# Kernel optimization log

Measured on AMD Instinct MI355X. Metric: run time of the kernel, lower is better.

Reference implementation:

```python
import jax, jax.numpy as jnp
import numpy as np

N_NODES = 100000


def gcn_conv(x, edge_index, W, b):
    # PyG GCNConv: linear first, then symmetric-normalized aggregation with self-loops, then bias.
    n = x.shape[0]
    h = x @ W  # [N, out]
    loop = jnp.arange(n, dtype=edge_index.dtype)
    src = jnp.concatenate([edge_index[0], loop])  # source nodes (x_j)
    dst = jnp.concatenate([edge_index[1], loop])  # target nodes (aggregation index)
    ones = jnp.ones(dst.shape[0], dtype=h.dtype)
    deg = jax.ops.segment_sum(ones, dst, num_segments=n)  # in-degree incl. self-loop
    dinv = jnp.where(deg > 0, jax.lax.rsqrt(deg), 0.0)
    norm = dinv[src] * dinv[dst]  # [E+N]
    msgs = h[src] * norm[:, None]  # gather + scale
    out = jax.ops.segment_sum(msgs, dst, num_segments=n)  # scatter-add
    return out + b


def setup_inputs() -> dict:
    key = jax.random.key(0)
    k1, k2, k3, k4 = jax.random.split(key, 4)
    x = jax.random.normal(k1, (N_NODES, 128), dtype=jnp.float32)
    edge_index = jax.random.randint(k2, (2, 3200000), 0, N_NODES, dtype=jnp.int64)
    W1 = jax.random.normal(k3, (128, 16), dtype=jnp.float32) * (1.0 / np.sqrt(128))
    b1 = jnp.zeros((16,), dtype=jnp.float32)
    W2 = jax.random.normal(k4, (16, 10), dtype=jnp.float32) * (1.0 / np.sqrt(16))
    b2 = jnp.zeros((10,), dtype=jnp.float32)
    return {"x": x, "edge_index": edge_index, "W1": W1, "b1": b1, "W2": W2, "b2": b2}


def reference(x, edge_index, W1, b1, W2, b2):
    h = gcn_conv(x, edge_index, W1, b1)
    h = jax.nn.relu(h)
    h = gcn_conv(h, edge_index, W2, b2)
    return jax.nn.log_softmax(h, axis=1)
```

## Files before the change

kernel.cpp:

```cpp
#include <hip/hip_runtime.h>
#include <hip/hip_fp16.h>
#include <math.h>

#define NN 100000
#define F0 128
#define F1 16
#define F2 10
#define NBUCK 391
#define TILE 8192
#define EPT 16
#define CAP 16384
#define BPT 512

__device__ inline void fma4(float4& a, float s, const float4& w) {
  a.x = fmaf(s, w.x, a.x);
  a.y = fmaf(s, w.y, a.y);
  a.z = fmaf(s, w.z, a.z);
  a.w = fmaf(s, w.w, a.w);
}

__device__ inline unsigned pk2(float a, float b) {
  __half ha = __float2half(a), hb = __float2half(b);
  return (unsigned)__half_as_ushort(ha) | ((unsigned)__half_as_ushort(hb) << 16);
}

__device__ inline float2 up2(unsigned u) {
  __half2 h;
  *(unsigned*)&h = u;
  return __half22float2(h);
}

__device__ inline void nt_store_f2(float a, float b, float* p) {
  union { double d; float f[2]; } u;
  u.f[0] = a; u.f[1] = b;
  __builtin_nontemporal_store(u.d, (double*)p);
}

__global__ void k_zero(int* __restrict__ bucket_cnt) {
  int i = blockIdx.x * blockDim.x + threadIdx.x;
  if (i < NBUCK) bucket_cnt[i] = 0;
}

__global__ __launch_bounds__(256) void k_bincount(const int* __restrict__ dst, int E,
                                                  int* __restrict__ bucket_cnt) {
  __shared__ int hist[NBUCK];
  int t = threadIdx.x;
  for (int i = t; i < NBUCK; i += 256) hist[i] = 0;
  __syncthreads();
  int per = (E + gridDim.x - 1) / gridDim.x;
  int e0 = blockIdx.x * per, e1 = min(E, e0 + per);
  for (int e = e0 + t; e < e1; e += 256)
    atomicAdd(&hist[__builtin_nontemporal_load(dst + e) >> 8], 1);
  __syncthreads();
  for (int i = t; i < NBUCK; i += 256)
    if (hist[i]) atomicAdd(&bucket_cnt[i], hist[i]);
}

__global__ void k_binscan(const int* __restrict__ bucket_cnt, int* __restrict__ bucket_base,
                          int* __restrict__ bucket_cur) {
  __shared__ int lds[512];
  int t = threadIdx.x;
  int v = (t < NBUCK) ? bucket_cnt[t] : 0;
  lds[t] = v;
  __syncthreads();
  for (int o = 1; o < 512; o <<= 1) {
    int add = (t >= o) ? lds[t - o] : 0;
    __syncthreads();
    lds[t] += add;
    __syncthreads();
  }
  if (t < NBUCK) {
    int excl = lds[t] - v;
    bucket_base[t] = excl;
    bucket_cur[t] = excl;
    if (t == NBUCK - 1) bucket_base[NBUCK] = lds[t];
  }
}

__global__ __launch_bounds__(BPT) void k_binplace(const int* __restrict__ src,
                                                  const int* __restrict__ dst, int E,
                                                  int* __restrict__ bucket_cur,
                                                  int* __restrict__ packed) {
  __shared__ int cnt[NBUCK];
  __shared__ int loff[NBUCK];
  __shared__ int gbase[NBUCK];
  __shared__ int part[256];
  __shared__ int stage[TILE];
  int t = threadIdx.x;
  int e0 = blockIdx.x * TILE, e1 = min(E, e0 + TILE);
  int total = e1 - e0;
  for (int i = t; i < NBUCK; i += BPT) cnt[i] = 0;
  __syncthreads();
  int bkpos[EPT];
  int pval[EPT];
#pragma unroll
  for (int k = 0; k < EPT; k++) {
    int e = e0 + t + k * BPT;
    if (e < e1) {
      int d = __builtin_nontemporal_load(dst + e);
      int s = __builtin_nontemporal_load(src + e);
      int bk = d >> 8;
      int pos = atomicAdd(&cnt[bk], 1);
      bkpos[k] = (bk << 13) | pos;
      pval[k] = (s << 8) | (d & 255);
    } else {
      bkpos[k] = -1;
    }
  }
  __syncthreads();
  for (int i = t; i < NBUCK; i += BPT) {
    int c = cnt[i];
    gbase[i] = c ? atomicAdd(&bucket_cur[i], c) : 0;
  }
  if (t < 256) {
    int i0 = 2 * t, i1 = 2 * t + 1;
    int c0 = (i0 < NBUCK) ? cnt[i0] : 0;
    int c1 = (i1 < NBUCK) ? cnt[i1] : 0;
    part[t] = c0 + c1;
  }
  __syncthreads();
  for (int o = 1; o < 256; o <<= 1) {
    int add = 0;
    if (t < 256 && t >= o) add = part[t - o];
    __syncthreads();
    if (t < 256) part[t] += add;
    __syncthreads();
  }
  if (t < 256) {
    int i0 = 2 * t, i1 = 2 * t + 1;
    int c0 = (i0 < NBUCK) ? cnt[i0] : 0;
    int c1 = (i1 < NBUCK) ? cnt[i1] : 0;
    int excl = part[t] - c0 - c1;
    if (i0 < NBUCK) loff[i0] = excl;
    if (i1 < NBUCK) loff[i1] = excl + c0;
  }
  __syncthreads();
#pragma unroll
  for (int k = 0; k < EPT; k++) {
    if (bkpos[k] >= 0) {
      int bk = bkpos[k] >> 13, pos = bkpos[k] & 8191;
      stage[loff[bk] + pos] = pval[k];
    }
  }
  __syncthreads();
  int sub = t >> 4, lane = t & 15;
  for (int bk = sub; bk < NBUCK; bk += BPT / 16) {
    int lo = loff[bk];
    int hi = (bk + 1 < NBUCK) ? loff[bk + 1] : total;
    int gb = gbase[bk];
    for (int i = lo + lane; i < hi; i += 16) packed[gb + (i - lo)] = stage[i];
  }
}

__global__ __launch_bounds__(256) void k_bucket(const int* __restrict__ packed,
                                                const int* __restrict__ bucket_base,
                                                int* __restrict__ row_start,
                                                float* __restrict__ dinv,
                                                int* __restrict__ col, int E) {
  __shared__ int stage[CAP];
  __shared__ int hist[256];
  __shared__ int off[256];
  __shared__ int cur[256];
  int b = blockIdx.x, t = threadIdx.x;
  int base = bucket_base[b];
  int cnt = bucket_base[b + 1] - base;
  hist[t] = 0;
  bool staged = (cnt <= CAP);
  if (staged)
    for (int i = t; i < cnt; i += 256) stage[i] = __builtin_nontemporal_load(packed + base + i);
  __syncthreads();
  if (staged) {
    for (int i = t; i < cnt; i += 256) atomicAdd(&hist[stage[i] & 255], 1);
  } else {
    for (int i = t; i < cnt; i += 256) atomicAdd(&hist[packed[base + i] & 255], 1);
  }
  __syncthreads();
  int v = hist[t];
  off[t] = v;
  __syncthreads();
  for (int o = 1; o < 256; o <<= 1) {
    int add = (t >= o) ? off[t - o] : 0;
    __syncthreads();
    off[t] += add;
    __syncthreads();
  }
  int excl = off[t] - v;
  cur[t] = excl;
  int d = b * 256 + t;
  if (d < NN) {
    row_start[d] = base + excl;
    dinv[d] = rsqrtf((float)(v + 1));
  }
  if (b == 0 && t == 0) row_start[NN] = E;
  __syncthreads();
  if (staged) {
    for (int i = t; i < cnt; i += 256) {
      int p = stage[i];
      int pos = atomicAdd(&cur[p & 255], 1);
      col[base + pos] = p >> 8;
    }
  } else {
    for (int i = t; i < cnt; i += 256) {
      int p = packed[base + i];
      int pos = atomicAdd(&cur[p & 255], 1);
      col[base + pos] = p >> 8;
    }
  }
}

__global__ __launch_bounds__(256) void k_lin1(const float* __restrict__ x,
                                              const float* __restrict__ W1,
                                              const float* __restrict__ dinv,
                                              unsigned* __restrict__ tab1) {
  __shared__ float4 wl[F0 * 4];
  int t = threadIdx.x;
  for (int i = t; i < F0 * 4; i += 256) wl[i] = ((const float4*)W1)[i];
  __syncthreads();
  int row0 = (blockIdx.x * 256 + t) * 4;
  if (row0 >= NN) return;
  float4 acc[4][4];
#pragma unroll
  for (int r = 0; r < 4; r++)
#pragma unroll
    for (int j = 0; j < 4; j++) acc[r][j] = make_float4(0.f, 0.f, 0.f, 0.f);
  const float4* xr0 = (const float4*)(x + (size_t)(row0 + 0) * F0);
  const float4* xr1 = (const float4*)(x + (size_t)(row0 + 1) * F0);
  const float4* xr2 = (const float4*)(x + (size_t)(row0 + 2) * F0);
  const float4* xr3 = (const float4*)(x + (size_t)(row0 + 3) * F0);
  for (int k4 = 0; k4 < F0 / 4; k4++) {
    float4 xv[4];
    xv[0] = xr0[k4]; xv[1] = xr1[k4]; xv[2] = xr2[k4]; xv[3] = xr3[k4];
#pragma unroll
    for (int kk = 0; kk < 4; kk++) {
      float4 w0 = wl[(k4 * 4 + kk) * 4 + 0];
      float4 w1 = wl[(k4 * 4 + kk) * 4 + 1];
      float4 w2 = wl[(k4 * 4 + kk) * 4 + 2];
      float4 w3 = wl[(k4 * 4 + kk) * 4 + 3];
#pragma unroll
      for (int r = 0; r < 4; r++) {
        float xs = kk == 0 ? xv[r].x : kk == 1 ? xv[r].y : kk == 2 ? xv[r].z : xv[r].w;
        fma4(acc[r][0], xs, w0);
        fma4(acc[r][1], xs, w1);
        fma4(acc[r][2], xs, w2);
        fma4(acc[r][3], xs, w3);
      }
    }
  }
#pragma unroll
  for (int r = 0; r < 4; r++) {
    float dd = dinv[row0 + r];
    float4 a0 = acc[r][0], a1 = acc[r][1], a2 = acc[r][2], a3 = acc[r][3];
    uint4 o0, o1;
    o0.x = pk2(dd * a0.x, dd * a0.y);
    o0.y = pk2(dd * a0.z, dd * a0.w);
    o0.z = pk2(dd * a1.x, dd * a1.y);
    o0.w = pk2(dd * a1.z, dd * a1.w);
    o1.x = pk2(dd * a2.x, dd * a2.y);
    o1.y = pk2(dd * a2.z, dd * a2.w);
    o1.z = pk2(dd * a3.x, dd * a3.y);
    o1.w = pk2(dd * a3.z, dd * a3.w);
    uint4* orow = (uint4*)(tab1 + (size_t)(row0 + r) * 8);
    orow[0] = o0;
    orow[1] = o1;
  }
}

__global__ __launch_bounds__(256) void k_agg1(const unsigned* __restrict__ tab1,
                                              const int* __restrict__ row_start,
                                              const int* __restrict__ col,
                                              const float* __restrict__ dinv,
                                              const float* __restrict__ b1,
                                              const float* __restrict__ W2g,
                                              unsigned* __restrict__ tab2) {
  __shared__ float w2[F1][F2];
  __shared__ float b1l[F1];
  int t = threadIdx.x;
  if (t < F1 * F2) w2[t / F2][t % F2] = W2g[t];
  if (t < F1) b1l[t] = b1[t];
  __syncthreads();
  int g = blockIdx.x * 256 + t;
  int d = g >> 3, o = g & 7;
  int q2 = o >> 2, q = o & 3;
  if (d >= NN) return;
  const uint2* T = (const uint2*)tab1;
  float a0 = 0.f, a1 = 0.f, a2 = 0.f, a3 = 0.f;
  auto addrow = [&](int s) {
    uint2 v = T[(size_t)s * 4 + q];
    float2 f0 = up2(v.x), f1 = up2(v.y);
    a0 += f0.x; a1 += f0.y; a2 += f1.x; a3 += f1.y;
  };
  if (q2 == 0) addrow(d);
  int e = row_start[d] + q2, e1 = row_start[d + 1];
  for (; e + 6 < e1; e += 8) {
    int s0 = __builtin_nontemporal_load(col + e);
    int s1 = __builtin_nontemporal_load(col + e + 2);
    int s2 = __builtin_nontemporal_load(col + e + 4);
    int s3 = __builtin_nontemporal_load(col + e + 6);
    addrow(s0); addrow(s1); addrow(s2); addrow(s3);
  }
  for (; e < e1; e += 2) addrow(__builtin_nontemporal_load(col + e));
  a0 += __shfl_xor(a0, 4);
  a1 += __shfl_xor(a1, 4);
  a2 += __shfl_xor(a2, 4);
  a3 += __shfl_xor(a3, 4);
  float dd = dinv[d];
  float h[4];
  h[0] = fmaxf(fmaf(dd, a0, b1l[q * 4 + 0]), 0.f);
  h[1] = fmaxf(fmaf(dd, a1, b1l[q * 4 + 1]), 0.f);
  h[2] = fmaxf(fmaf(dd, a2, b1l[q * 4 + 2]), 0.f);
  h[3] = fmaxf(fmaf(dd, a3, b1l[q * 4 + 3]), 0.f);
  float p[F2];
#pragma unroll
  for (int j = 0; j < F2; j++) {
    float s = 0.f;
#pragma unroll
    for (int kk = 0; kk < 4; kk++) s = fmaf(h[kk], w2[q * 4 + kk][j], s);
    p[j] = s;
  }
#pragma unroll
  for (int j = 0; j < F2; j++) p[j] += __shfl_xor(p[j], 1);
#pragma unroll
  for (int j = 0; j < F2; j++) p[j] += __shfl_xor(p[j], 2);
  if (q2 != 0) return;
  uint2* O = (uint2*)tab2;
  uint2 ov;
  if (q == 0) {
    ov.x = pk2(dd * p[0], dd * p[1]); ov.y = pk2(dd * p[2], dd * p[3]);
  } else if (q == 1) {
    ov.x = pk2(dd * p[4], dd * p[5]); ov.y = pk2(dd * p[6], dd * p[7]);
  } else if (q == 2) {
    ov.x = pk2(dd * p[8], dd * p[9]); ov.y = 0u;
  } else {
    ov.x = 0u; ov.y = 0u;
  }
  O[(size_t)d * 4 + q] = ov;
}

__global__ __launch_bounds__(256) void k_agg2(const unsigned* __restrict__ tab2,
                                              const int* __restrict__ row_start,
                                              const int* __restrict__ col,
                                              const float* __restrict__ dinv,
                                              const float* __restrict__ b2,
                                              float* __restrict__ out) {
  __shared__ float b2l[F1];
  int t = threadIdx.x;
  if (t < F1) b2l[t] = (t < F2) ? b2[t] : -1e30f;
  __syncthreads();
  int g = blockIdx.x * 256 + t;
  int d = g >> 3, o = g & 7;
  int q2 = o >> 2, q = o & 3;
  if (d >= NN) return;
  const uint2* T = (const uint2*)tab2;
  float a0 = 0.f, a1 = 0.f, a2 = 0.f, a3 = 0.f;
  auto addrow = [&](int s) {
    uint2 v = T[(size_t)s * 4 + q];
    float2 f0 = up2(v.x), f1 = up2(v.y);
    a0 += f0.x; a1 += f0.y; a2 += f1.x; a3 += f1.y;
  };
  if (q2 == 0) addrow(d);
  int e = row_start[d] + q2, e1 = row_start[d + 1];
  for (; e + 6 < e1; e += 8) {
    int s0 = __builtin_nontemporal_load(col + e);
    int s1 = __builtin_nontemporal_load(col + e + 2);
    int s2 = __builtin_nontemporal_load(col + e + 4);
    int s3 = __builtin_nontemporal_load(col + e + 6);
    addrow(s0); addrow(s1); addrow(s2); addrow(s3);
  }
  for (; e < e1; e += 2) addrow(__builtin_nontemporal_load(col + e));
  a0 += __shfl_xor(a0, 4);
  a1 += __shfl_xor(a1, 4);
  a2 += __shfl_xor(a2, 4);
  a3 += __shfl_xor(a3, 4);
  float dd = dinv[d];
  float v0 = fmaf(dd, a0, b2l[q * 4 + 0]);
  float v1 = fmaf(dd, a1, b2l[q * 4 + 1]);
  float v2 = fmaf(dd, a2, b2l[q * 4 + 2]);
  float v3 = fmaf(dd, a3, b2l[q * 4 + 3]);
  float m = fmaxf(fmaxf(v0, v1), fmaxf(v2, v3));
  m = fmaxf(m, __shfl_xor(m, 1));
  m = fmaxf(m, __shfl_xor(m, 2));
  float sum = expf(v0 - m) + expf(v1 - m) + expf(v2 - m) + expf(v3 - m);
  sum += __shfl_xor(sum, 1);
  sum += __shfl_xor(sum, 2);
  float lse = m + logf(sum);
  if (q2 != 0) return;
  float* op = out + (size_t)d * F2;
  if (q == 0) {
    nt_store_f2(v0 - lse, v1 - lse, op + 0);
    nt_store_f2(v2 - lse, v3 - lse, op + 2);
  } else if (q == 1) {
    nt_store_f2(v0 - lse, v1 - lse, op + 4);
    nt_store_f2(v2 - lse, v3 - lse, op + 6);
  } else if (q == 2) {
    nt_store_f2(v0 - lse, v1 - lse, op + 8);
  }
}

extern "C" void kernel_launch(void* const* d_in, const int* in_sizes, int n_in,
                              void* d_out, int out_size, void* d_ws, size_t ws_size,
                              hipStream_t stream) {
  const float* x  = (const float*)d_in[0];
  const int*   ei = (const int*)d_in[1];
  const float* W1 = (const float*)d_in[2];
  const float* b1 = (const float*)d_in[3];
  const float* W2 = (const float*)d_in[4];
  const float* b2 = (const float*)d_in[5];
  float* out = (float*)d_out;
  int E = in_sizes[1] / 2;
  const int* src = ei;
  const int* dst = ei + E;

  char* p = (char*)d_ws;
  auto alloc = [&](size_t bytes) {
    char* r = p;
    p += (bytes + 255) & ~(size_t)255;
    return r;
  };
  size_t tabsz = (size_t)NN * 8 * 4;
  float* dinv        = (float*)alloc((size_t)NN * 4);
  int*   row_start   = (int*)alloc((size_t)(NN + 1) * 4);
  int*   bucket_cnt  = (int*)alloc((size_t)NBUCK * 4);
  int*   bucket_base = (int*)alloc((size_t)(NBUCK + 1) * 4);
  int*   bucket_cur  = (int*)alloc((size_t)NBUCK * 4);
  int*   col         = (int*)alloc((size_t)E * 4);
  size_t needA = tabsz * 2;
  size_t regA = (size_t)E * 4;
  char*  A = (char*)alloc(regA > needA ? regA : needA);
  int*      packed = (int*)A;
  unsigned* tab1 = (unsigned*)A;
  unsigned* tab2 = (unsigned*)(A + tabsz);

  int nblk8N = (8 * NN + 255) / 256;
  int nblk_place = (E + TILE - 1) / TILE;
  hipLaunchKernelGGL(k_zero, dim3(2), dim3(256), 0, stream, bucket_cnt);
  hipLaunchKernelGGL(k_bincount, dim3(1024), dim3(256), 0, stream, dst, E, bucket_cnt);
  hipLaunchKernelGGL(k_binscan, dim3(1), dim3(512), 0, stream, bucket_cnt, bucket_base, bucket_cur);
  hipLaunchKernelGGL(k_binplace, dim3(nblk_place), dim3(BPT), 0, stream, src, dst, E, bucket_cur, packed);
  hipLaunchKernelGGL(k_bucket, dim3(NBUCK), dim3(256), 0, stream, packed, bucket_base, row_start, dinv, col, E);
  hipLaunchKernelGGL(k_lin1, dim3((NN / 4 + 255) / 256), dim3(256), 0, stream, x, W1, dinv, tab1);
  hipLaunchKernelGGL(k_agg1, dim3(nblk8N), dim3(256), 0, stream,
                     tab1, row_start, col, dinv, b1, W2, tab2);
  hipLaunchKernelGGL(k_agg2, dim3(nblk8N), dim3(256), 0, stream, tab2, row_start, col, dinv, b2, out);
}
```

Measured before the change: 197.7 us.

## Drop bucket-count pass by using fixed-capacity padded buckets with row_end

Removes the separate dst histogram and scan kernels by giving each destination bucket a fixed MAXB-sized slot in padded storage, so binplace reserves offsets directly through atomic counters. Rows are then described by row_start/row_end instead of a dense CSR offset array. k_bucket also records each edge's intra-node position during the histogram pass, which removes the second atomic pass when scattering columns. The cost is larger padded buffers, an extra row_end array, and a hard capacity assumption (MAXB) that can overflow if a bucket receives more edges than expected.

```diff
diff --git a/kernel.cpp b/kernel.cpp
--- a/kernel.cpp
+++ b/kernel.cpp
@@ -7,9 +7,10 @@
 #define F1 16
 #define F2 10
 #define NBUCK 391
+#define MAXB 10240
 #define TILE 8192
 #define EPT 16
-#define CAP 16384
+#define CAP 10240
 #define BPT 512
 
 __device__ inline void fma4(float4& a, float s, const float4& w) {
@@ -36,45 +37,9 @@
   __builtin_nontemporal_store(u.d, (double*)p);
 }
 
-__global__ void k_zero(int* __restrict__ bucket_cnt) {
+__global__ void k_zero(int* __restrict__ bucket_cur) {
   int i = blockIdx.x * blockDim.x + threadIdx.x;
-  if (i < NBUCK) bucket_cnt[i] = 0;
-}
-
-__global__ __launch_bounds__(256) void k_bincount(const int* __restrict__ dst, int E,
-                                                  int* __restrict__ bucket_cnt) {
-  __shared__ int hist[NBUCK];
-  int t = threadIdx.x;
-  for (int i = t; i < NBUCK; i += 256) hist[i] = 0;
-  __syncthreads();
-  int per = (E + gridDim.x - 1) / gridDim.x;
-  int e0 = blockIdx.x * per, e1 = min(E, e0 + per);
-  for (int e = e0 + t; e < e1; e += 256)
-    atomicAdd(&hist[__builtin_nontemporal_load(dst + e) >> 8], 1);
-  __syncthreads();
-  for (int i = t; i < NBUCK; i += 256)
-    if (hist[i]) atomicAdd(&bucket_cnt[i], hist[i]);
-}
-
-__global__ void k_binscan(const int* __restrict__ bucket_cnt, int* __restrict__ bucket_base,
-                          int* __restrict__ bucket_cur) {
-  __shared__ int lds[512];
-  int t = threadIdx.x;
-  int v = (t < NBUCK) ? bucket_cnt[t] : 0;
-  lds[t] = v;
-  __syncthreads();
-  for (int o = 1; o < 512; o <<= 1) {
-    int add = (t >= o) ? lds[t - o] : 0;
-    __syncthreads();
-    lds[t] += add;
-    __syncthreads();
-  }
-  if (t < NBUCK) {
-    int excl = lds[t] - v;
-    bucket_base[t] = excl;
-    bucket_cur[t] = excl;
-    if (t == NBUCK - 1) bucket_base[NBUCK] = lds[t];
-  }
+  if (i < NBUCK) bucket_cur[i] = 0;
 }
 
 __global__ __launch_bounds__(BPT) void k_binplace(const int* __restrict__ src,
@@ -147,60 +112,67 @@
   for (int bk = sub; bk < NBUCK; bk += BPT / 16) {
     int lo = loff[bk];
     int hi = (bk + 1 < NBUCK) ? loff[bk + 1] : total;
-    int gb = gbase[bk];
+    size_t gb = (size_t)bk * MAXB + gbase[bk];
     for (int i = lo + lane; i < hi; i += 16) packed[gb + (i - lo)] = stage[i];
   }
 }
 
 __global__ __launch_bounds__(256) void k_bucket(const int* __restrict__ packed,
-                                                const int* __restrict__ bucket_base,
+                                                const int* __restrict__ bucket_cur,
                                                 int* __restrict__ row_start,
+                                                int* __restrict__ row_end,
                                                 float* __restrict__ dinv,
-                                                int* __restrict__ col, int E) {
+                                                int* __restrict__ col) {
   __shared__ int stage[CAP];
+  __shared__ unsigned short posa[CAP];
   __shared__ int hist[256];
-  __shared__ int off[256];
+  __shared__ int offx[256];
+  __shared__ int scan[256];
   __shared__ int cur[256];
   int b = blockIdx.x, t = threadIdx.x;
-  int base = bucket_base[b];
-  int cnt = bucket_base[b + 1] - base;
+  size_t base = (size_t)b * MAXB;
+  int cnt_b = bucket_cur[b];
   hist[t] = 0;
-  bool staged = (cnt <= CAP);
-  if (staged)
-    for (int i = t; i < cnt; i += 256) stage[i] = __builtin_nontemporal_load(packed + base + i);
-  __syncthreads();
+  __syncthreads();
+  bool staged = (cnt_b <= CAP);
   if (staged) {
-    for (int i = t; i < cnt; i += 256) atomicAdd(&hist[stage[i] & 255], 1);
+    for (int i = t; i < cnt_b; i += 256) {
+      int p = __builtin_nontemporal_load(packed + base + i);
+      stage[i] = p;
+      int pos = atomicAdd(&hist[p & 255], 1);
+      posa[i] = (unsigned short)pos;
+    }
   } else {
-    for (int i = t; i < cnt; i += 256) atomicAdd(&hist[packed[base + i] & 255], 1);
+    for (int i = t; i < cnt_b; i += 256)
+      atomicAdd(&hist[packed[base + i] & 255], 1);
   }
   __syncthreads();
   int v = hist[t];
-  off[t] = v;
+  scan[t] = v;
   __syncthreads();
   for (int o = 1; o < 256; o <<= 1) {
-    int add = (t >= o) ? off[t - o] : 0;
+    int add = (t >= o) ? scan[t - o] : 0;
     __syncthreads();
-    off[t] += add;
+    scan[t] += add;
     __syncthreads();
   }
-  int excl = off[t] - v;
+  int excl = scan[t] - v;
+  offx[t] = excl;
   cur[t] = excl;
   int d = b * 256 + t;
   if (d < NN) {
-    row_start[d] = base + excl;
+    row_start[d] = (int)base + excl;
+    row_end[d] = (int)base + excl + v;
     dinv[d] = rsqrtf((float)(v + 1));
   }
-  if (b == 0 && t == 0) row_start[NN] = E;
   __syncthreads();
   if (staged) {
-    for (int i = t; i < cnt; i += 256) {
+    for (int i = t; i < cnt_b; i += 256) {
       int p = stage[i];
-      int pos = atomicAdd(&cur[p & 255], 1);
-      col[base + pos] = p >> 8;
+      col[base + offx[p & 255] + posa[i]] = p >> 8;
     }
   } else {
-    for (int i = t; i < cnt; i += 256) {
+    for (int i = t; i < cnt_b; i += 256) {
       int p = packed[base + i];
       int pos = atomicAdd(&cur[p & 255], 1);
       col[base + pos] = p >> 8;
@@ -267,6 +239,7 @@
 
 __global__ __launch_bounds__(256) void k_agg1(const unsigned* __restrict__ tab1,
                                               const int* __restrict__ row_start,
+                                              const int* __restrict__ row_end,
                                               const int* __restrict__ col,
                                               const float* __restrict__ dinv,
                                               const float* __restrict__ b1,
@@ -290,7 +263,7 @@
     a0 += f0.x; a1 += f0.y; a2 += f1.x; a3 += f1.y;
   };
   if (q2 == 0) addrow(d);
-  int e = row_start[d] + q2, e1 = row_start[d + 1];
+  int e = row_start[d] + q2, e1 = row_end[d];
   for (; e + 6 < e1; e += 8) {
     int s0 = __builtin_nontemporal_load(col + e);
     int s1 = __builtin_nontemporal_load(col + e + 2);
@@ -338,6 +311,7 @@
 
 __global__ __launch_bounds__(256) void k_agg2(const unsigned* __restrict__ tab2,
                                               const int* __restrict__ row_start,
+                                              const int* __restrict__ row_end,
                                               const int* __restrict__ col,
                                               const float* __restrict__ dinv,
                                               const float* __restrict__ b2,
@@ -358,7 +332,7 @@
     a0 += f0.x; a1 += f0.y; a2 += f1.x; a3 += f1.y;
   };
   if (q2 == 0) addrow(d);
-  int e = row_start[d] + q2, e1 = row_start[d + 1];
+  int e = row_start[d] + q2, e1 = row_end[d];
   for (; e + 6 < e1; e += 8) {
     int s0 = __builtin_nontemporal_load(col + e);
     int s1 = __builtin_nontemporal_load(col + e + 2);
@@ -417,28 +391,27 @@
     return r;
   };
   size_t tabsz = (size_t)NN * 8 * 4;
-  float* dinv        = (float*)alloc((size_t)NN * 4);
-  int*   row_start   = (int*)alloc((size_t)(NN + 1) * 4);
-  int*   bucket_cnt  = (int*)alloc((size_t)NBUCK * 4);
-  int*   bucket_base = (int*)alloc((size_t)(NBUCK + 1) * 4);
-  int*   bucket_cur  = (int*)alloc((size_t)NBUCK * 4);
-  int*   col         = (int*)alloc((size_t)E * 4);
-  size_t needA = tabsz * 2;
-  size_t regA = (size_t)E * 4;
-  char*  A = (char*)alloc(regA > needA ? regA : needA);
+  size_t padded = (size_t)NBUCK * MAXB * 4;
+  float* dinv       = (float*)alloc((size_t)NN * 4);
+  int*   row_start  = (int*)alloc((size_t)NN * 4);
+  int*   row_end    = (int*)alloc((size_t)NN * 4);
+  int*   bucket_cur = (int*)alloc((size_t)NBUCK * 4);
+  int*   col        = (int*)alloc(padded);
+  size_t needA = tabsz * 2 > padded ? tabsz * 2 : padded;
+  char*  A = (char*)alloc(needA);
   int*      packed = (int*)A;
   unsigned* tab1 = (unsigned*)A;
   unsigned* tab2 = (unsigned*)(A + tabsz);
 
   int nblk8N = (8 * NN + 255) / 256;
   int nblk_place = (E + TILE - 1) / TILE;
-  hipLaunchKernelGGL(k_zero, dim3(2), dim3(256), 0, stream, bucket_cnt);
-  hipLaunchKernelGGL(k_bincount, dim3(1024), dim3(256), 0, stream, dst, E, bucket_cnt);
-  hipLaunchKernelGGL(k_binscan, dim3(1), dim3(512), 0, stream, bucket_cnt, bucket_base, bucket_cur);
+  hipLaunchKernelGGL(k_zero, dim3(2), dim3(256), 0, stream, bucket_cur);
   hipLaunchKernelGGL(k_binplace, dim3(nblk_place), dim3(BPT), 0, stream, src, dst, E, bucket_cur, packed);
-  hipLaunchKernelGGL(k_bucket, dim3(NBUCK), dim3(256), 0, stream, packed, bucket_base, row_start, dinv, col, E);
+  hipLaunchKernelGGL(k_bucket, dim3(NBUCK), dim3(256), 0, stream,
+                     packed, bucket_cur, row_start, row_end, dinv, col);
   hipLaunchKernelGGL(k_lin1, dim3((NN / 4 + 255) / 256), dim3(256), 0, stream, x, W1, dinv, tab1);
   hipLaunchKernelGGL(k_agg1, dim3(nblk8N), dim3(256), 0, stream,
-                     tab1, row_start, col, dinv, b1, W2, tab2);
-  hipLaunchKernelGGL(k_agg2, dim3(nblk8N), dim3(256), 0, stream, tab2, row_start, col, dinv, b2, out);
-}
+                     tab1, row_start, row_end, col, dinv, b1, W2, tab2);
+  hipLaunchKernelGGL(k_agg2, dim3(nblk8N), dim3(256), 0, stream,
+                     tab2, row_start, row_end, col, dinv, b2, out);
+}
```

Measured after the change: 171.7 us. 1.15x faster.
